# Kernel optimization log

Measured on AMD Instinct MI355X. Metric: run time of the kernel, lower is better.

The kernel has to match this reference:

```python
import jax, jax.numpy as jnp
import numpy as np

B, C, HIMG, WIMG = 32, 3, 224, 224
P, D, L, F, H, NC = 16, 768, 12, 3072, 12, 1000
S = (HIMG // P) * (WIMG // P)  # 196 tokens
DH = D // H                    # 64 per head


def setup_inputs() -> dict:
    key = jax.random.key(0)
    ks = jax.random.split(key, 12)
    rn = lambda i, shape, sc: jax.random.normal(ks[i], shape, jnp.float32) * sc
    return dict(
        x=rn(0, (B, C, HIMG, WIMG), 1.0),
        conv_w=rn(1, (D, C, P, P), 0.02),
        conv_b=jnp.zeros((D,), jnp.float32),
        pos_embed=rn(2, (S, D), 0.02),
        ln1_s=jnp.ones((L, D), jnp.float32),
        ln1_b=jnp.zeros((L, D), jnp.float32),
        wq=rn(3, (L, D, D), 0.02),
        wk=rn(4, (L, D, D), 0.02),
        wv=rn(5, (L, D, D), 0.02),
        ln2_s=jnp.ones((L, D), jnp.float32),
        ln2_b=jnp.zeros((L, D), jnp.float32),
        w1=rn(6, (L, D, F), 0.02),
        b1=jnp.zeros((L, F), jnp.float32),
        w2=rn(7, (L, F, D), 0.02),
        b2=jnp.zeros((L, D), jnp.float32),
        fc_w=rn(8, (D, NC), 0.02),
        fc_b=jnp.zeros((NC,), jnp.float32),
    )


def _layernorm(x, scale, bias, eps=1e-5):
    m = x.mean(-1, keepdims=True)
    v = ((x - m) ** 2).mean(-1, keepdims=True)
    return (x - m) * jax.lax.rsqrt(v + eps) * scale + bias


def reference(x, conv_w, conv_b, pos_embed, ln1_s, ln1_b, wq, wk, wv,
              ln2_s, ln2_b, w1, b1, w2, b2, fc_w, fc_b):
    # patch embedding: stride-P conv, then b c h w -> b (h w) c, add pos embed
    h = jax.lax.conv_general_dilated(
        x, conv_w, (P, P), 'VALID',
        dimension_numbers=('NCHW', 'OIHW', 'NCHW'))
    h = h + conv_b[None, :, None, None]
    h = h.reshape(B, D, S).transpose(0, 2, 1) + pos_embed  # [B,S,D]

    # NOTE: original scales attention logits by 1/sqrt(seq_len), not 1/sqrt(d_head)
    scale = 1.0 / jnp.sqrt(jnp.float32(S))

    def layer(hx, p):
        l1s, l1b, Wq, Wk, Wv, l2s, l2b, W1, B1, W2, B2 = p
        xn = _layernorm(hx, l1s, l1b)
        q = (xn @ Wq).reshape(B, S, H, DH)
        k = (xn @ Wk).reshape(B, S, H, DH)
        v = (xn @ Wv).reshape(B, S, H, DH)
        att = jax.nn.softmax(jnp.einsum('bshd,bthd->bhst', q, k) * scale, axis=-1)
        o = jnp.einsum('bhst,bthd->bshd', att, v).reshape(B, S, D)
        hx = hx + o
        y = _layernorm(hx, l2s, l2b) @ W1 + B1
        y = jax.nn.gelu(y, approximate=False) @ W2 + B2
        return hx + y, None

    h, _ = jax.lax.scan(layer, h, (ln1_s, ln1_b, wq, wk, wv,
                                   ln2_s, ln2_b, w1, b1, w2, b2))
    return h.mean(axis=1) @ fc_w + fc_b  # [B, num_classes]
```

## Files before the change

### kernel.cpp

```cpp
#include <hip/hip_runtime.h>
#include <hip/hip_bf16.h>

typedef __attribute__((ext_vector_type(8))) short bf16x8;
typedef __attribute__((ext_vector_type(4))) short bf16x4;
typedef __attribute__((ext_vector_type(4))) float f32x4;

#define DEVI static __device__ __forceinline__

DEVI unsigned short f2bf(float f) {
  __hip_bfloat16 h = __float2bfloat16(f);
  return __builtin_bit_cast(unsigned short, h);
}

DEVI f32x4 mfma16(bf16x8 a, bf16x8 b, f32x4 c) {
  return __builtin_amdgcn_mfma_f32_16x16x32_bf16(a, b, c, 0, 0, 0);
}

DEVI void gload16(const unsigned short* g, unsigned short* l) {
  __builtin_amdgcn_global_load_lds(
      (const __attribute__((address_space(1))) void*)g,
      (__attribute__((address_space(3))) void*)l, 16, 0, 0);
}

DEVI float erf_fast(float x) {
  float ax = fabsf(x);
  float t = 1.f / (1.f + 0.3275911f * ax);
  float poly = ((((1.061405429f * t - 1.453152027f) * t + 1.421413741f) * t -
                 0.284496736f) * t + 0.254829592f) * t;
  float e = __expf(-x * x);
  float er = 1.f - poly * e;
  return copysignf(er, x);
}

__global__ __launch_bounds__(256) void k_im2col(const float* __restrict__ x,
                                                unsigned short* __restrict__ A) {
  int t = blockIdx.x * 256 + threadIdx.x;
  int m = t / 192;
  int qq = t - m * 192;
  int kk = qq * 4;
  int c = kk >> 8;
  int r = kk & 255;
  int i = r >> 4;
  int j = r & 15;
  int b = m / 196;
  int s = m - b * 196;
  int ph = s / 14;
  int pw = s - ph * 14;
  const float* src = x + ((size_t)((b * 3 + c) * 224 + ph * 16 + i)) * 224 + pw * 16 + j;
  f32x4 v = *reinterpret_cast<const f32x4*>(src);
  bf16x4 o;
  o[0] = (short)f2bf(v[0]); o[1] = (short)f2bf(v[1]);
  o[2] = (short)f2bf(v[2]); o[3] = (short)f2bf(v[3]);
  *reinterpret_cast<bf16x4*>(A + (size_t)m * 768 + kk) = o;
}

__global__ __launch_bounds__(256) void k_cvt(const float* __restrict__ in,
                                             unsigned short* __restrict__ out) {
  int t = blockIdx.x * 256 + threadIdx.x;
  f32x4 v = *reinterpret_cast<const f32x4*>(in + (size_t)t * 4);
  bf16x4 o;
  o[0] = (short)f2bf(v[0]); o[1] = (short)f2bf(v[1]);
  o[2] = (short)f2bf(v[2]); o[3] = (short)f2bf(v[3]);
  *reinterpret_cast<bf16x4*>(out + (size_t)t * 4) = o;
}

DEVI void transpose_tile(const float* __restrict__ in, unsigned short* __restrict__ out,
                         int K, int N, int kt, int nt, unsigned short (*tile)[68]) {
  int r = threadIdx.x >> 4;
  int c4 = (threadIdx.x & 15) * 4;
  int k0 = kt * 64, n0 = nt * 64;
#pragma unroll
  for (int rr0 = 0; rr0 < 4; rr0++) {
    int rr = r + rr0 * 16;
    f32x4 v = *reinterpret_cast<const f32x4*>(in + (size_t)(k0 + rr) * N + n0 + c4);
    bf16x4 o;
    o[0] = (short)f2bf(v[0]); o[1] = (short)f2bf(v[1]);
    o[2] = (short)f2bf(v[2]); o[3] = (short)f2bf(v[3]);
    *reinterpret_cast<bf16x4*>(&tile[rr][c4]) = o;
  }
  __syncthreads();
#pragma unroll
  for (int rr0 = 0; rr0 < 4; rr0++) {
    int rr = r + rr0 * 16;
    bf16x4 o;
    o[0] = (short)tile[c4 + 0][rr];
    o[1] = (short)tile[c4 + 1][rr];
    o[2] = (short)tile[c4 + 2][rr];
    o[3] = (short)tile[c4 + 3][rr];
    *reinterpret_cast<bf16x4*>(out + (size_t)(n0 + rr) * K + k0 + c4) = o;
  }
}

__global__ __launch_bounds__(256) void k_wconvert(
    const float* __restrict__ wq, const float* __restrict__ wk, const float* __restrict__ wv,
    const float* __restrict__ w1, const float* __restrict__ w2,
    unsigned short* __restrict__ wqkvT, unsigned short* __restrict__ w1T,
    unsigned short* __restrict__ w2T) {
  __shared__ unsigned short tile[64][68];
  int bid = blockIdx.x;
  if (bid < 432) {
    int mm = bid / 144, t2 = bid - mm * 144;
    const float* in = (mm == 0) ? wq : ((mm == 1) ? wk : wv);
    transpose_tile(in, wqkvT + (size_t)mm * 768 * 768, 768, 768, t2 / 12, t2 % 12, tile);
  } else if (bid < 1008) {
    int t2 = bid - 432;
    transpose_tile(w1, w1T, 768, 3072, t2 / 48, t2 % 48, tile);
  } else {
    int t2 = bid - 1008;
    transpose_tile(w2, w2T, 3072, 768, t2 / 12, t2 % 12, tile);
  }
}

__global__ __launch_bounds__(256) void k_ln(const float* __restrict__ h,
                                            const float* __restrict__ sc,
                                            const float* __restrict__ bi,
                                            unsigned short* __restrict__ xn) {
  int wave = threadIdx.x >> 6, lane = threadIdx.x & 63;
  int row = blockIdx.x * 4 + wave;
  const float* hr = h + (size_t)row * 768;
  f32x4 v[3];
  float sum = 0.f;
#pragma unroll
  for (int i = 0; i < 3; i++) {
    v[i] = *reinterpret_cast<const f32x4*>(hr + i * 256 + lane * 4);
    sum += v[i][0] + v[i][1] + v[i][2] + v[i][3];
  }
#pragma unroll
  for (int m = 1; m < 64; m <<= 1) sum += __shfl_xor(sum, m, 64);
  float mean = sum * (1.f / 768.f);
  float var = 0.f;
#pragma unroll
  for (int i = 0; i < 3; i++)
#pragma unroll
    for (int c = 0; c < 4; c++) { float d = v[i][c] - mean; var += d * d; }
#pragma unroll
  for (int m = 1; m < 64; m <<= 1) var += __shfl_xor(var, m, 64);
  float rs = rsqrtf(var * (1.f / 768.f) + 1e-5f);
#pragma unroll
  for (int i = 0; i < 3; i++) {
    int col = i * 256 + lane * 4;
    f32x4 s4 = *reinterpret_cast<const f32x4*>(sc + col);
    f32x4 b4 = *reinterpret_cast<const f32x4*>(bi + col);
    bf16x4 o;
#pragma unroll
    for (int c = 0; c < 4; c++) o[c] = (short)f2bf((v[i][c] - mean) * rs * s4[c] + b4[c]);
    *reinterpret_cast<bf16x4*>(xn + (size_t)row * 768 + col) = o;
  }
}

template <int EPI>
__global__ __launch_bounds__(256) void k_gemm(
    const unsigned short* __restrict__ A, const unsigned short* __restrict__ Bt, int K,
    const float* __restrict__ bias, const float* __restrict__ aux,
    float* __restrict__ outF, unsigned short* __restrict__ outB) {
  __shared__ __align__(16) unsigned short As[2][128 * 32];
  __shared__ __align__(16) unsigned short Bs[2][128 * 32];

  int GX = gridDim.x, GY = gridDim.y;
  int nb = GX * GY;
  int lin = blockIdx.y * GX + blockIdx.x;
  int q = nb >> 3, r8 = nb & 7;
  int xcd = lin & 7, off = lin >> 3;
  int wid = (xcd < r8 ? xcd * (q + 1) : r8 * (q + 1) + (xcd - r8) * q) + off;
  const int GM = 8;
  int per = GM * GX;
  int g = wid / per;
  int first_m = g * GM;
  int gm = min(GM, GY - first_m);
  int rem = wid - g * per;
  int mt = first_m + rem % gm;
  int nt = rem / gm;
  int m0 = mt * 128, n0 = nt * 128;

  int tid = threadIdx.x;
  int wave = tid >> 6, lane = tid & 63;
  int wm = (wave >> 1) * 64, wn = (wave & 1) * 64;
  int lr = lane & 15, lg = lane >> 4;

  f32x4 acc[4][4];
  const f32x4 fz = {0.f, 0.f, 0.f, 0.f};
#pragma unroll
  for (int i = 0; i < 4; i++)
#pragma unroll
    for (int j = 0; j < 4; j++) acc[i][j] = fz;

  int srow = wave * 16 + (lane >> 2);
  int scol = (lane & 3) * 8;
  const unsigned short* Ag = A + (size_t)(m0 + srow) * K + scol;
  const unsigned short* Bg = Bt + (size_t)(n0 + srow) * K + scol;
  int lofs = wave * 16 * 32;

  int nk = K >> 5;
#pragma unroll
  for (int j = 0; j < 2; j++) {
    gload16(Ag + (size_t)j * 64 * K, &As[0][lofs + j * 64 * 32]);
    gload16(Bg + (size_t)j * 64 * K, &Bs[0][lofs + j * 64 * 32]);
  }
  __syncthreads();

  for (int kt = 0; kt < nk - 1; kt++) {
    int cur = kt & 1;
    int k0 = (kt + 1) << 5;
#pragma unroll
    for (int j = 0; j < 2; j++) {
      gload16(Ag + (size_t)j * 64 * K + k0, &As[cur ^ 1][lofs + j * 64 * 32]);
      gload16(Bg + (size_t)j * 64 * K + k0, &Bs[cur ^ 1][lofs + j * 64 * 32]);
    }
    bf16x8 a[4], b[4];
#pragma unroll
    for (int i = 0; i < 4; i++) {
      a[i] = *reinterpret_cast<const bf16x8*>(&As[cur][(wm + i * 16 + lr) * 32 + lg * 8]);
      b[i] = *reinterpret_cast<const bf16x8*>(&Bs[cur][(wn + i * 16 + lr) * 32 + lg * 8]);
    }
#pragma unroll
    for (int mi = 0; mi < 4; mi++)
#pragma unroll
      for (int ni = 0; ni < 4; ni++) acc[mi][ni] = mfma16(a[mi], b[ni], acc[mi][ni]);
    __syncthreads();
  }
  {
    int cur = (nk - 1) & 1;
    bf16x8 a[4], b[4];
#pragma unroll
    for (int i = 0; i < 4; i++) {
      a[i] = *reinterpret_cast<const bf16x8*>(&As[cur][(wm + i * 16 + lr) * 32 + lg * 8]);
      b[i] = *reinterpret_cast<const bf16x8*>(&Bs[cur][(wn + i * 16 + lr) * 32 + lg * 8]);
    }
#pragma unroll
    for (int mi = 0; mi < 4; mi++)
#pragma unroll
      for (int ni = 0; ni < 4; ni++) acc[mi][ni] = mfma16(a[mi], b[ni], acc[mi][ni]);
  }

  if (EPI == 1) {
#pragma unroll
    for (int ni = 0; ni < 4; ni++) {
      int n = n0 + wn + ni * 16 + lr;
      int which = (n >= 1536) ? 2 : ((n >= 768) ? 1 : 0);
      int n7 = n - which * 768;
      int hd = n7 >> 6, dh = n7 & 63;
      unsigned short* ob = outB + (size_t)which * 4816896 + dh;
#pragma unroll
      for (int mi = 0; mi < 4; mi++) {
        int mb = m0 + wm + mi * 16 + lg * 4;
        int bb = mb / 196;
        int s = mb - bb * 196;
#pragma unroll
        for (int r = 0; r < 4; r++) {
          ob[((size_t)((bb * 12 + hd) * 196 + s) << 6)] = f2bf(acc[mi][ni][r]);
          s++;
          if (s == 196) { s = 0; bb++; }
        }
      }
    }
  } else {
#pragma unroll
    for (int mi = 0; mi < 4; mi++) {
      int mb = m0 + wm + mi * 16 + lg * 4;
      int bb = mb / 196;
      int s0 = mb - bb * 196;
#pragma unroll
      for (int ni = 0; ni < 4; ni++) {
        int n = n0 + wn + ni * 16 + lr;
        int s = s0;
#pragma unroll
        for (int r = 0; r < 4; r++) {
          int m = mb + r;
          float val = acc[mi][ni][r];
          if (EPI == 0) {
            outF[(size_t)m * 768 + n] = val + bias[n] + aux[(size_t)s * 768 + n];
            s++;
            if (s == 196) s = 0;
          } else if (EPI == 2) {
            float u = val + bias[n];
            float gg = 0.5f * u * (1.f + erf_fast(u * 0.70710678118654752f));
            outB[(size_t)m * 3072 + n] = f2bf(gg);
          } else {
            outF[(size_t)m * 768 + n] += val + bias[n];
          }
        }
      }
    }
  }
}

__global__ __launch_bounds__(256) void k_attn(const unsigned short* __restrict__ q,
                                              const unsigned short* __restrict__ k,
                                              const unsigned short* __restrict__ v,
                                              float* __restrict__ h) {
  __shared__ __align__(16) unsigned short Kl[208][72];
  __shared__ __align__(16) unsigned short Vt[64][248];
  __shared__ __align__(16) unsigned short Sc[4][16][232];
  int bh = blockIdx.x;
  int b = bh / 12, hh = bh - b * 12;
  size_t base = (size_t)bh * 196 * 64;
  int tid = threadIdx.x, wave = tid >> 6, lane = tid & 63;
  int lr = lane & 15, lg = lane >> 4;

  const bf16x8 bz = {0, 0, 0, 0, 0, 0, 0, 0};
  for (int u = tid; u < 208 * 8; u += 256) {
    int row = u >> 3, c8 = (u & 7) * 8;
    bf16x8 val = bz;
    if (row < 196) val = *reinterpret_cast<const bf16x8*>(k + base + row * 64 + c8);
    *reinterpret_cast<bf16x8*>(&Kl[row][c8]) = val;
  }
  for (int u = tid; u < 224 * 8; u += 256) {
    int t = u >> 3, d8 = (u & 7) * 8;
    bf16x8 val = bz;
    if (t < 196) val = *reinterpret_cast<const bf16x8*>(v + base + t * 64 + d8);
#pragma unroll
    for (int i = 0; i < 8; i++) Vt[d8 + i][t] = (unsigned short)val[i];
  }
  for (int i2 = lane; i2 < 256; i2 += 64) Sc[wave][i2 >> 4][208 + (i2 & 15)] = 0;
  __syncthreads();

  const float scale = 1.f / 14.f;
  for (int st = wave; st < 13; st += 4) {
    int qb = st * 16;
    int s = qb + lr;
    bf16x8 aq0 = bz, aq1 = bz;
    if (s < 196) {
      aq0 = *reinterpret_cast<const bf16x8*>(q + base + (size_t)s * 64 + lg * 8);
      aq1 = *reinterpret_cast<const bf16x8*>(q + base + (size_t)s * 64 + 32 + lg * 8);
    }
    f32x4 sc[13];
#pragma unroll
    for (int t = 0; t < 13; t++) {
      bf16x8 bk0 = *reinterpret_cast<const bf16x8*>(&Kl[t * 16 + lr][lg * 8]);
      bf16x8 bk1 = *reinterpret_cast<const bf16x8*>(&Kl[t * 16 + lr][32 + lg * 8]);
      f32x4 z = {0.f, 0.f, 0.f, 0.f};
      z = mfma16(aq0, bk0, z);
      z = mfma16(aq1, bk1, z);
      sc[t] = z;
    }
    float mx[4] = {-1e30f, -1e30f, -1e30f, -1e30f};
#pragma unroll
    for (int t = 0; t < 13; t++) {
      int tc = t * 16 + lr;
#pragma unroll
      for (int r = 0; r < 4; r++) {
        float xv = (tc < 196) ? sc[t][r] * scale : -1e30f;
        sc[t][r] = xv;
        mx[r] = fmaxf(mx[r], xv);
      }
    }
#pragma unroll
    for (int r = 0; r < 4; r++)
#pragma unroll
      for (int mm = 1; mm < 16; mm <<= 1) mx[r] = fmaxf(mx[r], __shfl_xor(mx[r], mm, 64));
    float sm[4] = {0.f, 0.f, 0.f, 0.f};
#pragma unroll
    for (int t = 0; t < 13; t++)
#pragma unroll
      for (int r = 0; r < 4; r++) {
        float e = __expf(sc[t][r] - mx[r]);
        sc[t][r] = e;
        sm[r] += e;
      }
#pragma unroll
    for (int r = 0; r < 4; r++)
#pragma unroll
      for (int mm = 1; mm < 16; mm <<= 1) sm[r] += __shfl_xor(sm[r], mm, 64);
    float inv[4];
#pragma unroll
    for (int r = 0; r < 4; r++) inv[r] = 1.f / sm[r];
#pragma unroll
    for (int t = 0; t < 13; t++)
#pragma unroll
      for (int r = 0; r < 4; r++)
        Sc[wave][lg * 4 + r][t * 16 + lr] = f2bf(sc[t][r] * inv[r]);
    asm volatile("s_waitcnt lgkmcnt(0)" ::: "memory");
    bf16x8 ap[7];
#pragma unroll
    for (int ks = 0; ks < 7; ks++)
      ap[ks] = *reinterpret_cast<const bf16x8*>(&Sc[wave][lr][ks * 32 + lg * 8]);
#pragma unroll
    for (int nt = 0; nt < 4; nt++) {
      f32x4 o = {0.f, 0.f, 0.f, 0.f};
#pragma unroll
      for (int ks = 0; ks < 7; ks++) {
        bf16x8 bv = *reinterpret_cast<const bf16x8*>(&Vt[nt * 16 + lr][ks * 32 + lg * 8]);
        o = mfma16(ap[ks], bv, o);
      }
#pragma unroll
      for (int r = 0; r < 4; r++) {
        int s2 = qb + lg * 4 + r;
        if (s2 < 196) h[(size_t)(b * 196 + s2) * 768 + hh * 64 + nt * 16 + lr] += o[r];
      }
    }
  }
}

__global__ __launch_bounds__(256) void k_mean(const float* __restrict__ h,
                                              float* __restrict__ hm) {
  int b = blockIdx.x, d = blockIdx.y * 256 + threadIdx.x;
  float acc = 0.f;
  for (int s = 0; s < 196; s++) acc += h[(size_t)(b * 196 + s) * 768 + d];
  hm[b * 768 + d] = acc * (1.f / 196.f);
}

__global__ __launch_bounds__(256) void k_fc(const float* __restrict__ hm,
                                            const float* __restrict__ w,
                                            const float* __restrict__ bias,
                                            float* __restrict__ out) {
  int b = blockIdx.x, n = blockIdx.y * 256 + threadIdx.x;
  if (n >= 1000) return;
  float acc = bias[n];
  for (int d = 0; d < 768; d++) acc += hm[b * 768 + d] * w[d * 1000 + n];
  out[b * 1000 + n] = acc;
}

extern "C" void kernel_launch(void* const* d_in, const int* in_sizes, int n_in,
                              void* d_out, int out_size, void* d_ws, size_t ws_size,
                              hipStream_t stream) {
  const float* x      = (const float*)d_in[0];
  const float* conv_w = (const float*)d_in[1];
  const float* conv_b = (const float*)d_in[2];
  const float* pos    = (const float*)d_in[3];
  const float* ln1_s  = (const float*)d_in[4];
  const float* ln1_b  = (const float*)d_in[5];
  const float* wq     = (const float*)d_in[6];
  const float* wk     = (const float*)d_in[7];
  const float* wv     = (const float*)d_in[8];
  const float* ln2_s  = (const float*)d_in[9];
  const float* ln2_b  = (const float*)d_in[10];
  const float* w1     = (const float*)d_in[11];
  const float* b1     = (const float*)d_in[12];
  const float* w2     = (const float*)d_in[13];
  const float* b2     = (const float*)d_in[14];
  const float* fc_w   = (const float*)d_in[15];
  const float* fc_b   = (const float*)d_in[16];
  float* out = (float*)d_out;

  char* p = (char*)d_ws;
  auto alloc = [&](size_t bytes) {
    char* r = p;
    p += (bytes + 255) & ~(size_t)255;
    return r;
  };
  const size_t M = 6272, QSZ = 4816896;
  float* h              = (float*)alloc(M * 768 * 4);
  unsigned short* xn    = (unsigned short*)alloc(M * 768 * 2);
  unsigned short* qkv   = (unsigned short*)alloc(3 * QSZ * 2);
  unsigned short* y1    = (unsigned short*)alloc(M * 3072 * 2);
  unsigned short* wqkvT = (unsigned short*)alloc((size_t)2304 * 768 * 2);
  unsigned short* w1T   = (unsigned short*)alloc((size_t)3072 * 768 * 2);
  unsigned short* w2T   = (unsigned short*)alloc((size_t)3072 * 768 * 2);
  unsigned short* cwB   = (unsigned short*)alloc((size_t)768 * 768 * 2);
  float* hm             = (float*)alloc(32 * 768 * 4);

  k_cvt<<<576, 256, 0, stream>>>(conv_w, cwB);
  k_im2col<<<4704, 256, 0, stream>>>(x, xn);
  k_gemm<0><<<dim3(6, 49), 256, 0, stream>>>(xn, cwB, 768, conv_b, pos, h, nullptr);

  for (int l = 0; l < 12; l++) {
    k_wconvert<<<1584, 256, 0, stream>>>(
        wq + (size_t)l * 589824, wk + (size_t)l * 589824, wv + (size_t)l * 589824,
        w1 + (size_t)l * 2359296, w2 + (size_t)l * 2359296, wqkvT, w1T, w2T);
    k_ln<<<1568, 256, 0, stream>>>(h, ln1_s + l * 768, ln1_b + l * 768, xn);
    k_gemm<1><<<dim3(18, 49), 256, 0, stream>>>(xn, wqkvT, 768, nullptr, nullptr, nullptr, qkv);
    k_attn<<<384, 256, 0, stream>>>(qkv, qkv + QSZ, qkv + 2 * QSZ, h);
    k_ln<<<1568, 256, 0, stream>>>(h, ln2_s + l * 768, ln2_b + l * 768, xn);
    k_gemm<2><<<dim3(24, 49), 256, 0, stream>>>(xn, w1T, 768, b1 + (size_t)l * 3072, nullptr,
                                                nullptr, y1);
    k_gemm<3><<<dim3(6, 49), 256, 0, stream>>>(y1, w2T, 3072, b2 + (size_t)l * 768, nullptr, h,
                                               nullptr);
  }
  k_mean<<<dim3(32, 3), 256, 0, stream>>>(h, hm);
  k_fc<<<dim3(32, 4), 256, 0, stream>>>(hm, fc_w, fc_b, out);
}
```

Baseline: 3.274 ms.

## Add 256x256 tile GEMM with XCD-aware swizzle for QKV and MLP layers

Adds a new 512-thread GEMM kernel with 256x256 output tiles, 64-wide K steps, XOR-swizzled LDS layout, double-buffered direct global-to-LDS loads, and a block remap that groups tiles per XCD and by M-groups for L2 reuse. It is used for the QKV, FC1 and FC2 GEMMs, while the old kernel stays only for the patch embedding. Activation buffers are padded to 6400 rows so tiles can read past M without bounds checks, and the epilogue skips invalid rows. The larger tiles raise arithmetic intensity, at the cost of fewer blocks: FC2 gets only 75 blocks, which can underfill the GPU. The conv weight buffer now aliases the qkv buffer.

```diff
diff --git a/kernel.cpp b/kernel.cpp
--- a/kernel.cpp
+++ b/kernel.cpp
@@ -232,17 +232,140 @@
       for (int ni = 0; ni < 4; ni++) acc[mi][ni] = mfma16(a[mi], b[ni], acc[mi][ni]);
   }
 
-  if (EPI == 1) {
+#pragma unroll
+  for (int mi = 0; mi < 4; mi++) {
+    int mb = m0 + wm + mi * 16 + lg * 4;
+    int bb = mb / 196;
+    int s0 = mb - bb * 196;
 #pragma unroll
     for (int ni = 0; ni < 4; ni++) {
       int n = n0 + wn + ni * 16 + lr;
+      int s = s0;
+#pragma unroll
+      for (int r = 0; r < 4; r++) {
+        int m = mb + r;
+        float val = acc[mi][ni][r];
+        outF[(size_t)m * 768 + n] = val + bias[n] + aux[(size_t)s * 768 + n];
+        s++;
+        if (s == 196) s = 0;
+      }
+    }
+  }
+}
+
+template <int EPI>
+__global__ __launch_bounds__(512) void k_gemm256(
+    const unsigned short* __restrict__ A, const unsigned short* __restrict__ Bt, int K,
+    const float* __restrict__ bias, float* __restrict__ outF,
+    unsigned short* __restrict__ outB) {
+  __shared__ __align__(16) unsigned short As[2][16384];
+  __shared__ __align__(16) unsigned short Bs[2][16384];
+  const int MVALID = 6272;
+
+  int GX = gridDim.x, GY = gridDim.y;
+  int nb = GX * GY;
+  int lin = blockIdx.y * GX + blockIdx.x;
+  int q = nb >> 3, r8 = nb & 7;
+  int xcd = lin & 7, off = lin >> 3;
+  int wid = (xcd < r8 ? xcd * (q + 1) : r8 * (q + 1) + (xcd - r8) * q) + off;
+  const int GM = 8;
+  int per = GM * GX;
+  int g = wid / per;
+  int first_m = g * GM;
+  int gm = min(GM, GY - first_m);
+  int rem = wid - g * per;
+  int mt = first_m + rem % gm;
+  int nt = rem / gm;
+  int m0 = mt * 256, n0 = nt * 256;
+
+  int tid = threadIdx.x;
+  int w = tid >> 6, lane = tid & 63;
+  int wm2 = w >> 2, wn4 = w & 3;
+  int lr = lane & 15, lg = lane >> 4;
+
+  f32x4 acc[8][4];
+  const f32x4 fz = {0.f, 0.f, 0.f, 0.f};
+#pragma unroll
+  for (int i = 0; i < 8; i++)
+#pragma unroll
+    for (int j = 0; j < 4; j++) acc[i][j] = fz;
+
+  int srow = w * 8 + (lane >> 3);
+  int scole = ((lane & 7) ^ (lane >> 3)) * 8;
+  const unsigned short* Ag = A + (size_t)(m0 + srow) * K + scole;
+  const unsigned short* Bg = Bt + (size_t)(n0 + srow) * K + scole;
+
+  int lofsA = wm2 * 8192 + lr * 64;
+  int lofsB = (wn4 >> 1) * 8192 + ((wn4 & 1) * 64 + lr) * 64;
+  int swz = (lr & 7) << 3;
+  int colk0 = (lg * 8) ^ swz;
+  int colk1 = (32 + lg * 8) ^ swz;
+
+  int nk = K >> 6;
+
+#define STAGE256(kt, buf)                                                      \
+  {                                                                            \
+    const unsigned short* a_ = Ag + (size_t)(kt) * 64;                         \
+    const unsigned short* b_ = Bg + (size_t)(kt) * 64;                         \
+    _Pragma("unroll") for (int h_ = 0; h_ < 2; h_++)                           \
+        _Pragma("unroll") for (int j_ = 0; j_ < 2; j_++) {                     \
+      size_t go_ = (size_t)(h_ * 128 + j_ * 64) * K;                           \
+      int lo_ = h_ * 8192 + (j_ * 8 + w) * 512;                                \
+      gload16(a_ + go_, &As[buf][lo_]);                                        \
+      gload16(b_ + go_, &Bs[buf][lo_]);                                        \
+    }                                                                          \
+  }
+
+#define COMPUTE256(buf)                                                        \
+  {                                                                            \
+    _Pragma("unroll") for (int ks = 0; ks < 2; ks++) {                         \
+      int ca = (ks == 0) ? colk0 : colk1;                                      \
+      bf16x8 bfr[4];                                                           \
+      _Pragma("unroll") for (int ni = 0; ni < 4; ni++) bfr[ni] =               \
+          *reinterpret_cast<const bf16x8*>(&Bs[buf][lofsB + ni * 1024 + ca]);  \
+      _Pragma("unroll") for (int mi = 0; mi < 8; mi++) {                       \
+        bf16x8 afr =                                                           \
+            *reinterpret_cast<const bf16x8*>(&As[buf][lofsA + mi * 1024 + ca]); \
+        _Pragma("unroll") for (int ni = 0; ni < 4; ni++) acc[mi][ni] =         \
+            mfma16(afr, bfr[ni], acc[mi][ni]);                                 \
+      }                                                                        \
+    }                                                                          \
+  }
+
+  STAGE256(0, 0);
+  STAGE256(1, 1);
+  asm volatile("s_waitcnt vmcnt(8)" ::: "memory");
+  __builtin_amdgcn_s_barrier();
+
+  for (int kt = 0; kt < nk; kt++) {
+    int cur = kt & 1;
+    COMPUTE256(cur);
+    asm volatile("s_waitcnt lgkmcnt(0)" ::: "memory");
+    __builtin_amdgcn_s_barrier();
+    if (kt + 2 < nk) {
+      STAGE256(kt + 2, cur);
+      asm volatile("s_waitcnt vmcnt(8)" ::: "memory");
+      __builtin_amdgcn_s_barrier();
+    } else if (kt + 1 < nk) {
+      asm volatile("s_waitcnt vmcnt(0)" ::: "memory");
+      __builtin_amdgcn_s_barrier();
+    }
+  }
+#undef STAGE256
+#undef COMPUTE256
+
+  if (EPI == 1) {
+#pragma unroll
+    for (int ni = 0; ni < 4; ni++) {
+      int n = n0 + wn4 * 64 + ni * 16 + lr;
       int which = (n >= 1536) ? 2 : ((n >= 768) ? 1 : 0);
       int n7 = n - which * 768;
       int hd = n7 >> 6, dh = n7 & 63;
       unsigned short* ob = outB + (size_t)which * 4816896 + dh;
 #pragma unroll
-      for (int mi = 0; mi < 4; mi++) {
-        int mb = m0 + wm + mi * 16 + lg * 4;
+      for (int mi = 0; mi < 8; mi++) {
+        int mb = m0 + wm2 * 128 + mi * 16 + lg * 4;
+        if (mb >= MVALID) continue;
         int bb = mb / 196;
         int s = mb - bb * 196;
 #pragma unroll
@@ -255,23 +378,17 @@
     }
   } else {
 #pragma unroll
-    for (int mi = 0; mi < 4; mi++) {
-      int mb = m0 + wm + mi * 16 + lg * 4;
-      int bb = mb / 196;
-      int s0 = mb - bb * 196;
+    for (int mi = 0; mi < 8; mi++) {
+      int mb = m0 + wm2 * 128 + mi * 16 + lg * 4;
+      if (mb >= MVALID) continue;
 #pragma unroll
       for (int ni = 0; ni < 4; ni++) {
-        int n = n0 + wn + ni * 16 + lr;
-        int s = s0;
+        int n = n0 + wn4 * 64 + ni * 16 + lr;
 #pragma unroll
         for (int r = 0; r < 4; r++) {
           int m = mb + r;
           float val = acc[mi][ni][r];
-          if (EPI == 0) {
-            outF[(size_t)m * 768 + n] = val + bias[n] + aux[(size_t)s * 768 + n];
-            s++;
-            if (s == 196) s = 0;
-          } else if (EPI == 2) {
+          if (EPI == 2) {
             float u = val + bias[n];
             float gg = 0.5f * u * (1.f + erf_fast(u * 0.70710678118654752f));
             outB[(size_t)m * 3072 + n] = f2bf(gg);
@@ -438,16 +555,16 @@
     p += (bytes + 255) & ~(size_t)255;
     return r;
   };
-  const size_t M = 6272, QSZ = 4816896;
+  const size_t M = 6272, MP = 6400, QSZ = 4816896;
   float* h              = (float*)alloc(M * 768 * 4);
-  unsigned short* xn    = (unsigned short*)alloc(M * 768 * 2);
+  unsigned short* xn    = (unsigned short*)alloc(MP * 768 * 2);
   unsigned short* qkv   = (unsigned short*)alloc(3 * QSZ * 2);
-  unsigned short* y1    = (unsigned short*)alloc(M * 3072 * 2);
+  unsigned short* y1    = (unsigned short*)alloc(MP * 3072 * 2);
   unsigned short* wqkvT = (unsigned short*)alloc((size_t)2304 * 768 * 2);
   unsigned short* w1T   = (unsigned short*)alloc((size_t)3072 * 768 * 2);
   unsigned short* w2T   = (unsigned short*)alloc((size_t)3072 * 768 * 2);
-  unsigned short* cwB   = (unsigned short*)alloc((size_t)768 * 768 * 2);
   float* hm             = (float*)alloc(32 * 768 * 4);
+  unsigned short* cwB   = qkv;
 
   k_cvt<<<576, 256, 0, stream>>>(conv_w, cwB);
   k_im2col<<<4704, 256, 0, stream>>>(x, xn);
@@ -458,13 +575,13 @@
         wq + (size_t)l * 589824, wk + (size_t)l * 589824, wv + (size_t)l * 589824,
         w1 + (size_t)l * 2359296, w2 + (size_t)l * 2359296, wqkvT, w1T, w2T);
     k_ln<<<1568, 256, 0, stream>>>(h, ln1_s + l * 768, ln1_b + l * 768, xn);
-    k_gemm<1><<<dim3(18, 49), 256, 0, stream>>>(xn, wqkvT, 768, nullptr, nullptr, nullptr, qkv);
+    k_gemm256<1><<<dim3(9, 25), 512, 0, stream>>>(xn, wqkvT, 768, nullptr, nullptr, qkv);
     k_attn<<<384, 256, 0, stream>>>(qkv, qkv + QSZ, qkv + 2 * QSZ, h);
     k_ln<<<1568, 256, 0, stream>>>(h, ln2_s + l * 768, ln2_b + l * 768, xn);
-    k_gemm<2><<<dim3(24, 49), 256, 0, stream>>>(xn, w1T, 768, b1 + (size_t)l * 3072, nullptr,
-                                                nullptr, y1);
-    k_gemm<3><<<dim3(6, 49), 256, 0, stream>>>(y1, w2T, 3072, b2 + (size_t)l * 768, nullptr, h,
-                                               nullptr);
+    k_gemm256<2><<<dim3(12, 25), 512, 0, stream>>>(xn, w1T, 768, b1 + (size_t)l * 3072,
+                                                   nullptr, y1);
+    k_gemm256<3><<<dim3(3, 25), 512, 0, stream>>>(y1, w2T, 3072, b2 + (size_t)l * 768, h,
+                                                  nullptr);
   }
   k_mean<<<dim3(32, 3), 256, 0, stream>>>(h, hm);
   k_fc<<<dim3(32, 4), 256, 0, stream>>>(hm, fc_w, fc_b, out);
```

New measurement: 3.572 ms. +9.1%, slower.

## Use 256x256 tiled GEMM with triple-buffered LDS and split-K atomics for MLP

Applied to the files above, without the earlier changes.

Replaces the 128x128 double-buffered GEMM for the QKV, FC1 and FC2 layers with a 512-thread, 256x256-tile kernel. It uses three LDS stages with explicit waitcnt and barrier control and raises wave priority around the MFMA block. Rows are padded to 6400 and the FC2 GEMM is split three ways along K, accumulating into the residual with atomicAdd. Larger tiles give more data reuse per load and the split restores parallelism for the narrow FC2 output. In exchange, atomics make FC2 accumulation order nondeterministic, padded rows do wasted work, and the larger tiles use more registers and LDS.

```diff
diff --git a/kernel.cpp b/kernel.cpp
--- a/kernel.cpp
+++ b/kernel.cpp
@@ -148,30 +148,14 @@
   }
 }
 
-template <int EPI>
-__global__ __launch_bounds__(256) void k_gemm(
+__global__ __launch_bounds__(256) void k_gemm_patch(
     const unsigned short* __restrict__ A, const unsigned short* __restrict__ Bt, int K,
     const float* __restrict__ bias, const float* __restrict__ aux,
-    float* __restrict__ outF, unsigned short* __restrict__ outB) {
+    float* __restrict__ outF) {
   __shared__ __align__(16) unsigned short As[2][128 * 32];
   __shared__ __align__(16) unsigned short Bs[2][128 * 32];
 
-  int GX = gridDim.x, GY = gridDim.y;
-  int nb = GX * GY;
-  int lin = blockIdx.y * GX + blockIdx.x;
-  int q = nb >> 3, r8 = nb & 7;
-  int xcd = lin & 7, off = lin >> 3;
-  int wid = (xcd < r8 ? xcd * (q + 1) : r8 * (q + 1) + (xcd - r8) * q) + off;
-  const int GM = 8;
-  int per = GM * GX;
-  int g = wid / per;
-  int first_m = g * GM;
-  int gm = min(GM, GY - first_m);
-  int rem = wid - g * per;
-  int mt = first_m + rem % gm;
-  int nt = rem / gm;
-  int m0 = mt * 128, n0 = nt * 128;
-
+  int m0 = blockIdx.y * 128, n0 = blockIdx.x * 128;
   int tid = threadIdx.x;
   int wave = tid >> 6, lane = tid & 63;
   int wm = (wave >> 1) * 64, wn = (wave & 1) * 64;
@@ -232,17 +216,136 @@
       for (int ni = 0; ni < 4; ni++) acc[mi][ni] = mfma16(a[mi], b[ni], acc[mi][ni]);
   }
 
-  if (EPI == 1) {
+#pragma unroll
+  for (int mi = 0; mi < 4; mi++) {
+    int mb = m0 + wm + mi * 16 + lg * 4;
+    int bb = mb / 196;
+    int s0 = mb - bb * 196;
 #pragma unroll
     for (int ni = 0; ni < 4; ni++) {
       int n = n0 + wn + ni * 16 + lr;
+      int s = s0;
+#pragma unroll
+      for (int r = 0; r < 4; r++) {
+        int m = mb + r;
+        outF[(size_t)m * 768 + n] = acc[mi][ni][r] + bias[n] + aux[(size_t)s * 768 + n];
+        s++;
+        if (s == 196) s = 0;
+      }
+    }
+  }
+}
+
+template <int EPI>
+__global__ __launch_bounds__(512) void k_gemm256(
+    const unsigned short* __restrict__ A, const unsigned short* __restrict__ Bt,
+    int K, int nk, const float* __restrict__ bias, float* __restrict__ outF,
+    unsigned short* __restrict__ outB) {
+  __shared__ __align__(16) unsigned short As[3][8192];
+  __shared__ __align__(16) unsigned short Bs[3][8192];
+  const int MVALID = 6272;
+
+  int GX = gridDim.x, GY = gridDim.y, GZ = gridDim.z;
+  int nb = GX * GY * GZ;
+  int lin = (blockIdx.z * GY + blockIdx.y) * GX + blockIdx.x;
+  int q = nb >> 3, r8 = nb & 7;
+  int xcd = lin & 7, off = lin >> 3;
+  int wid = (xcd < r8 ? xcd * (q + 1) : r8 * (q + 1) + (xcd - r8) * q) + off;
+  int t2 = GX * GY;
+  int sz = wid / t2;
+  int w2 = wid - sz * t2;
+  const int GM = 4;
+  int per = GM * GX;
+  int g = w2 / per;
+  int first_m = g * GM;
+  int gm = min(GM, GY - first_m);
+  int rem = w2 - g * per;
+  int mt = first_m + rem % gm;
+  int nt = rem / gm;
+  int m0 = mt * 256, n0 = nt * 256;
+  int kb = sz * nk;
+
+  int tid = threadIdx.x;
+  int w = tid >> 6, lane = tid & 63;
+  int wm2 = w >> 2, wn4 = w & 3;
+  int lr = lane & 15, lg = lane >> 4;
+
+  f32x4 acc[8][4];
+  const f32x4 fz = {0.f, 0.f, 0.f, 0.f};
+#pragma unroll
+  for (int i = 0; i < 8; i++)
+#pragma unroll
+    for (int j = 0; j < 4; j++) acc[i][j] = fz;
+
+  const unsigned short* Ag =
+      A + (size_t)(m0 + (lane >> 2)) * K + (lane & 3) * 8 + (size_t)kb * 32;
+  const unsigned short* Bg =
+      Bt + (size_t)(n0 + (lane >> 2)) * K + (lane & 3) * 8 + (size_t)kb * 32;
+
+  int lofsA = wm2 * 4096 + lr * 32 + lg * 8;
+  int lofsB = wn4 * 2048 + lr * 32 + lg * 8;
+
+#define STAGE32(kt, la, lb)                                                    \
+  {                                                                            \
+    const unsigned short* a_ = Ag + (size_t)(kt) * 32;                         \
+    const unsigned short* b_ = Bg + (size_t)(kt) * 32;                         \
+    gload16(a_ + (size_t)w * 16 * K, (la) + w * 512);                          \
+    gload16(a_ + (size_t)(w + 8) * 16 * K, (la) + (w + 8) * 512);              \
+    gload16(b_ + (size_t)w * 16 * K, (lb) + w * 512);                          \
+    gload16(b_ + (size_t)(w + 8) * 16 * K, (lb) + (w + 8) * 512);              \
+  }
+
+#define COMPUTE32(pa, pb)                                                      \
+  {                                                                            \
+    bf16x8 afr[8], bfr[4];                                                     \
+    _Pragma("unroll") for (int ni = 0; ni < 4; ni++) bfr[ni] =                 \
+        *reinterpret_cast<const bf16x8*>((pb) + lofsB + ni * 512);             \
+    _Pragma("unroll") for (int mi = 0; mi < 8; mi++) afr[mi] =                 \
+        *reinterpret_cast<const bf16x8*>((pa) + lofsA + mi * 512);             \
+    __builtin_amdgcn_s_setprio(1);                                             \
+    _Pragma("unroll") for (int mi = 0; mi < 8; mi++)                           \
+        _Pragma("unroll") for (int ni = 0; ni < 4; ni++) acc[mi][ni] =         \
+            mfma16(afr[mi], bfr[ni], acc[mi][ni]);                             \
+    __builtin_amdgcn_s_setprio(0);                                             \
+  }
+
+  unsigned short* pa0 = &As[0][0]; unsigned short* pb0 = &Bs[0][0];
+  unsigned short* pa1 = &As[1][0]; unsigned short* pb1 = &Bs[1][0];
+  unsigned short* pa2 = &As[2][0]; unsigned short* pb2 = &Bs[2][0];
+
+  STAGE32(0, pa0, pb0);
+  STAGE32(1, pa1, pb1);
+
+  for (int kt = 0; kt < nk - 1; kt++) {
+    asm volatile("s_waitcnt lgkmcnt(0)" ::: "memory");
+    asm volatile("s_waitcnt vmcnt(4)" ::: "memory");
+    __builtin_amdgcn_s_barrier();
+    __builtin_amdgcn_sched_barrier(0);
+    if (kt + 2 < nk) STAGE32(kt + 2, pa2, pb2);
+    COMPUTE32(pa0, pb0);
+    unsigned short* ta = pa0; pa0 = pa1; pa1 = pa2; pa2 = ta;
+    unsigned short* tb = pb0; pb0 = pb1; pb1 = pb2; pb2 = tb;
+  }
+  asm volatile("s_waitcnt lgkmcnt(0)" ::: "memory");
+  asm volatile("s_waitcnt vmcnt(0)" ::: "memory");
+  __builtin_amdgcn_s_barrier();
+  __builtin_amdgcn_sched_barrier(0);
+  COMPUTE32(pa0, pb0);
+#undef STAGE32
+#undef COMPUTE32
+
+  if (EPI == 1) {
+#pragma unroll
+    for (int ni = 0; ni < 4; ni++) {
+      int n = n0 + wn4 * 64 + ni * 16 + lr;
       int which = (n >= 1536) ? 2 : ((n >= 768) ? 1 : 0);
       int n7 = n - which * 768;
       int hd = n7 >> 6, dh = n7 & 63;
       unsigned short* ob = outB + (size_t)which * 4816896 + dh;
 #pragma unroll
-      for (int mi = 0; mi < 4; mi++) {
-        int mb = m0 + wm + mi * 16 + lg * 4;
+      for (int mi = 0; mi < 8; mi++) {
+        int mb = m0 + wm2 * 128 + mi * 16 + lg * 4;
+        if (mb >= MVALID) continue;
         int bb = mb / 196;
         int s = mb - bb * 196;
 #pragma unroll
@@ -255,28 +358,23 @@
     }
   } else {
 #pragma unroll
-    for (int mi = 0; mi < 4; mi++) {
-      int mb = m0 + wm + mi * 16 + lg * 4;
-      int bb = mb / 196;
-      int s0 = mb - bb * 196;
+    for (int mi = 0; mi < 8; mi++) {
+      int mb = m0 + wm2 * 128 + mi * 16 + lg * 4;
+      if (mb >= MVALID) continue;
 #pragma unroll
       for (int ni = 0; ni < 4; ni++) {
-        int n = n0 + wn + ni * 16 + lr;
-        int s = s0;
+        int n = n0 + wn4 * 64 + ni * 16 + lr;
 #pragma unroll
         for (int r = 0; r < 4; r++) {
           int m = mb + r;
           float val = acc[mi][ni][r];
-          if (EPI == 0) {
-            outF[(size_t)m * 768 + n] = val + bias[n] + aux[(size_t)s * 768 + n];
-            s++;
-            if (s == 196) s = 0;
-          } else if (EPI == 2) {
+          if (EPI == 2) {
             float u = val + bias[n];
             float gg = 0.5f * u * (1.f + erf_fast(u * 0.70710678118654752f));
             outB[(size_t)m * 3072 + n] = f2bf(gg);
           } else {
-            outF[(size_t)m * 768 + n] += val + bias[n];
+            float bn = (sz == 0) ? bias[n] : 0.f;
+            atomicAdd(&outF[(size_t)m * 768 + n], val + bn);
           }
         }
       }
@@ -438,33 +536,34 @@
     p += (bytes + 255) & ~(size_t)255;
     return r;
   };
-  const size_t M = 6272, QSZ = 4816896;
+  const size_t M = 6272, MP = 6400, QSZ = 4816896;
   float* h              = (float*)alloc(M * 768 * 4);
-  unsigned short* xn    = (unsigned short*)alloc(M * 768 * 2);
+  unsigned short* xn    = (unsigned short*)alloc(MP * 768 * 2);
   unsigned short* qkv   = (unsigned short*)alloc(3 * QSZ * 2);
-  unsigned short* y1    = (unsigned short*)alloc(M * 3072 * 2);
+  unsigned short* y1    = (unsigned short*)alloc(MP * 3072 * 2);
   unsigned short* wqkvT = (unsigned short*)alloc((size_t)2304 * 768 * 2);
   unsigned short* w1T   = (unsigned short*)alloc((size_t)3072 * 768 * 2);
   unsigned short* w2T   = (unsigned short*)alloc((size_t)3072 * 768 * 2);
-  unsigned short* cwB   = (unsigned short*)alloc((size_t)768 * 768 * 2);
   float* hm             = (float*)alloc(32 * 768 * 4);
+  unsigned short* cwB   = qkv;
 
   k_cvt<<<576, 256, 0, stream>>>(conv_w, cwB);
   k_im2col<<<4704, 256, 0, stream>>>(x, xn);
-  k_gemm<0><<<dim3(6, 49), 256, 0, stream>>>(xn, cwB, 768, conv_b, pos, h, nullptr);
+  k_gemm_patch<<<dim3(6, 49), 256, 0, stream>>>(xn, cwB, 768, conv_b, pos, h);
 
   for (int l = 0; l < 12; l++) {
     k_wconvert<<<1584, 256, 0, stream>>>(
         wq + (size_t)l * 589824, wk + (size_t)l * 589824, wv + (size_t)l * 589824,
         w1 + (size_t)l * 2359296, w2 + (size_t)l * 2359296, wqkvT, w1T, w2T);
     k_ln<<<1568, 256, 0, stream>>>(h, ln1_s + l * 768, ln1_b + l * 768, xn);
-    k_gemm<1><<<dim3(18, 49), 256, 0, stream>>>(xn, wqkvT, 768, nullptr, nullptr, nullptr, qkv);
+    k_gemm256<1><<<dim3(9, 25, 1), 512, 0, stream>>>(xn, wqkvT, 768, 24, nullptr, nullptr,
+                                                     qkv);
     k_attn<<<384, 256, 0, stream>>>(qkv, qkv + QSZ, qkv + 2 * QSZ, h);
     k_ln<<<1568, 256, 0, stream>>>(h, ln2_s + l * 768, ln2_b + l * 768, xn);
-    k_gemm<2><<<dim3(24, 49), 256, 0, stream>>>(xn, w1T, 768, b1 + (size_t)l * 3072, nullptr,
-                                                nullptr, y1);
-    k_gemm<3><<<dim3(6, 49), 256, 0, stream>>>(y1, w2T, 3072, b2 + (size_t)l * 768, nullptr, h,
-                                               nullptr);
+    k_gemm256<2><<<dim3(12, 25, 1), 512, 0, stream>>>(xn, w1T, 768, 24,
+                                                      b1 + (size_t)l * 3072, nullptr, y1);
+    k_gemm256<3><<<dim3(3, 25, 3), 512, 0, stream>>>(y1, w2T, 3072, 32,
+                                                     b2 + (size_t)l * 768, h, nullptr);
   }
   k_mean<<<dim3(32, 3), 256, 0, stream>>>(h, hm);
   k_fc<<<dim3(32, 4), 256, 0, stream>>>(hm, fc_w, fc_b, out);
```

Result: slower. 3.797 ms (+16.0%).

## Add 256x256 4-stage pipelined GEMM for QKV and FC1 projections

Applied to the files above, without the earlier changes.

Adds a new 512-thread GEMM kernel with 256x256 output tiles, a 4-deep global_load_lds ring buffer, swizzled LDS layout, XCD-aware block remapping with grouped M ordering, and s_setprio around the MFMA bursts. The QKV and FC1 GEMMs switch to it, and the original kernel keeps only the conv and FC2 epilogues. The xn and y1 buffers are padded to 6400 rows so the last M tile can read past the valid 6272 rows, and stores to those rows are skipped. The aim is more operand reuse per LDS load and better latency hiding. In exchange the kernel uses more registers and LDS and wastes some compute on padding rows. The conv weight buffer now aliases the qkv buffer.

```diff
diff --git a/kernel.cpp b/kernel.cpp
--- a/kernel.cpp
+++ b/kernel.cpp
@@ -232,17 +232,136 @@
       for (int ni = 0; ni < 4; ni++) acc[mi][ni] = mfma16(a[mi], b[ni], acc[mi][ni]);
   }
 
-  if (EPI == 1) {
+#pragma unroll
+  for (int mi = 0; mi < 4; mi++) {
+    int mb = m0 + wm + mi * 16 + lg * 4;
+    int bb = mb / 196;
+    int s0 = mb - bb * 196;
 #pragma unroll
     for (int ni = 0; ni < 4; ni++) {
       int n = n0 + wn + ni * 16 + lr;
+      int s = s0;
+#pragma unroll
+      for (int r = 0; r < 4; r++) {
+        int m = mb + r;
+        float val = acc[mi][ni][r];
+        if (EPI == 0) {
+          outF[(size_t)m * 768 + n] = val + bias[n] + aux[(size_t)s * 768 + n];
+          s++;
+          if (s == 196) s = 0;
+        } else {
+          outF[(size_t)m * 768 + n] += val + bias[n];
+        }
+      }
+    }
+  }
+}
+
+template <int EPI>
+__global__ __launch_bounds__(512, 2) void k_gemm256p(
+    const unsigned short* __restrict__ A, const unsigned short* __restrict__ Bt,
+    const float* __restrict__ bias, unsigned short* __restrict__ outB) {
+  const int K = 768, NK = 24;
+  __shared__ __align__(16) unsigned short LDS[4][16384];
+  const int MVALID = 6272;
+
+  int GX = gridDim.x, GY = gridDim.y;
+  int nb = GX * GY;
+  int lin = blockIdx.y * GX + blockIdx.x;
+  int q = nb >> 3, r8 = nb & 7;
+  int xcd = lin & 7, off = lin >> 3;
+  int wid = (xcd < r8 ? xcd * (q + 1) : r8 * (q + 1) + (xcd - r8) * q) + off;
+  const int GM = 4;
+  int per = GM * GX;
+  int g = wid / per;
+  int first_m = g * GM;
+  int gm = min(GM, GY - first_m);
+  int rem = wid - g * per;
+  int mt = first_m + rem % gm;
+  int nt = rem / gm;
+  int m0 = mt * 256, n0 = nt * 256;
+
+  int tid = threadIdx.x;
+  int w = tid >> 6, lane = tid & 63;
+  int wm = w >> 2, wn = w & 3;
+  int lr = lane & 15, lg = lane >> 4;
+
+  f32x4 acc[8][4];
+  const f32x4 fz = {0.f, 0.f, 0.f, 0.f};
+#pragma unroll
+  for (int i = 0; i < 8; i++)
+#pragma unroll
+    for (int j = 0; j < 4; j++) acc[i][j] = fz;
+
+  int srow = w * 16 + (lane >> 2);
+  int scol = ((lane & 3) ^ ((lane >> 3) & 3)) * 8;
+  const unsigned short* Ag = A + (size_t)(m0 + srow) * K + scol;
+  const unsigned short* Bg = Bt + (size_t)(n0 + srow) * K + scol;
+  int ldst = w * 512;
+
+  int colsw = (lg ^ ((lr >> 1) & 3)) * 8;
+  int rofA = wm * 4096 + lr * 32 + colsw;
+  int rofB = 8192 + wn * 2048 + lr * 32 + colsw;
+
+#define STAGEP(kt)                                                          \
+  {                                                                         \
+    unsigned short* d_ = &LDS[(kt) & 3][0];                                 \
+    const unsigned short* a_ = Ag + (kt) * 32;                              \
+    const unsigned short* b_ = Bg + (kt) * 32;                              \
+    gload16(a_, d_ + ldst);                                                 \
+    gload16(a_ + (size_t)128 * K, d_ + 4096 + ldst);                        \
+    gload16(b_, d_ + 8192 + ldst);                                          \
+    gload16(b_ + (size_t)128 * K, d_ + 12288 + ldst);                       \
+  }
+
+  STAGEP(0);
+  STAGEP(1);
+  STAGEP(2);
+  asm volatile("s_waitcnt vmcnt(8)" ::: "memory");
+  __builtin_amdgcn_s_barrier();
+
+  for (int kt = 0; kt < NK; kt++) {
+    if (kt + 3 < NK) STAGEP(kt + 3);
+    const unsigned short* bufA = &LDS[kt & 3][0];
+    bf16x8 a[8], b[4];
+#pragma unroll
+    for (int ni = 0; ni < 4; ni++)
+      b[ni] = *reinterpret_cast<const bf16x8*>(bufA + rofB + ni * 512);
+#pragma unroll
+    for (int mi = 0; mi < 8; mi++)
+      a[mi] = *reinterpret_cast<const bf16x8*>(bufA + rofA + mi * 512);
+    __builtin_amdgcn_s_setprio(1);
+#pragma unroll
+    for (int mi = 0; mi < 8; mi++)
+#pragma unroll
+      for (int ni = 0; ni < 4; ni++) acc[mi][ni] = mfma16(a[mi], b[ni], acc[mi][ni]);
+    __builtin_amdgcn_s_setprio(0);
+    if (kt + 1 < NK) {
+      asm volatile("s_waitcnt lgkmcnt(0)" ::: "memory");
+      if (kt + 3 < NK) {
+        asm volatile("s_waitcnt vmcnt(8)" ::: "memory");
+      } else if (kt + 2 < NK) {
+        asm volatile("s_waitcnt vmcnt(4)" ::: "memory");
+      } else {
+        asm volatile("s_waitcnt vmcnt(0)" ::: "memory");
+      }
+      __builtin_amdgcn_s_barrier();
+    }
+  }
+#undef STAGEP
+
+  if (EPI == 1) {
+#pragma unroll
+    for (int ni = 0; ni < 4; ni++) {
+      int n = n0 + wn * 64 + ni * 16 + lr;
       int which = (n >= 1536) ? 2 : ((n >= 768) ? 1 : 0);
       int n7 = n - which * 768;
       int hd = n7 >> 6, dh = n7 & 63;
       unsigned short* ob = outB + (size_t)which * 4816896 + dh;
 #pragma unroll
-      for (int mi = 0; mi < 4; mi++) {
-        int mb = m0 + wm + mi * 16 + lg * 4;
+      for (int mi = 0; mi < 8; mi++) {
+        int mb = m0 + wm * 128 + mi * 16 + lg * 4;
+        if (mb >= MVALID) continue;
         int bb = mb / 196;
         int s = mb - bb * 196;
 #pragma unroll
@@ -255,29 +374,18 @@
     }
   } else {
 #pragma unroll
-    for (int mi = 0; mi < 4; mi++) {
-      int mb = m0 + wm + mi * 16 + lg * 4;
-      int bb = mb / 196;
-      int s0 = mb - bb * 196;
+    for (int mi = 0; mi < 8; mi++) {
+      int mb = m0 + wm * 128 + mi * 16 + lg * 4;
+      if (mb >= MVALID) continue;
 #pragma unroll
       for (int ni = 0; ni < 4; ni++) {
-        int n = n0 + wn + ni * 16 + lr;
-        int s = s0;
+        int n = n0 + wn * 64 + ni * 16 + lr;
 #pragma unroll
         for (int r = 0; r < 4; r++) {
           int m = mb + r;
-          float val = acc[mi][ni][r];
-          if (EPI == 0) {
-            outF[(size_t)m * 768 + n] = val + bias[n] + aux[(size_t)s * 768 + n];
-            s++;
-            if (s == 196) s = 0;
-          } else if (EPI == 2) {
-            float u = val + bias[n];
-            float gg = 0.5f * u * (1.f + erf_fast(u * 0.70710678118654752f));
-            outB[(size_t)m * 3072 + n] = f2bf(gg);
-          } else {
-            outF[(size_t)m * 768 + n] += val + bias[n];
-          }
+          float u = acc[mi][ni][r] + bias[n];
+          float gg = 0.5f * u * (1.f + erf_fast(u * 0.70710678118654752f));
+          outB[(size_t)m * 3072 + n] = f2bf(gg);
         }
       }
     }
@@ -438,16 +546,16 @@
     p += (bytes + 255) & ~(size_t)255;
     return r;
   };
-  const size_t M = 6272, QSZ = 4816896;
+  const size_t M = 6272, MP = 6400, QSZ = 4816896;
   float* h              = (float*)alloc(M * 768 * 4);
-  unsigned short* xn    = (unsigned short*)alloc(M * 768 * 2);
+  unsigned short* xn    = (unsigned short*)alloc(MP * 768 * 2);
   unsigned short* qkv   = (unsigned short*)alloc(3 * QSZ * 2);
-  unsigned short* y1    = (unsigned short*)alloc(M * 3072 * 2);
+  unsigned short* y1    = (unsigned short*)alloc(MP * 3072 * 2);
   unsigned short* wqkvT = (unsigned short*)alloc((size_t)2304 * 768 * 2);
   unsigned short* w1T   = (unsigned short*)alloc((size_t)3072 * 768 * 2);
   unsigned short* w2T   = (unsigned short*)alloc((size_t)3072 * 768 * 2);
-  unsigned short* cwB   = (unsigned short*)alloc((size_t)768 * 768 * 2);
   float* hm             = (float*)alloc(32 * 768 * 4);
+  unsigned short* cwB   = qkv;
 
   k_cvt<<<576, 256, 0, stream>>>(conv_w, cwB);
   k_im2col<<<4704, 256, 0, stream>>>(x, xn);
@@ -458,13 +566,12 @@
         wq + (size_t)l * 589824, wk + (size_t)l * 589824, wv + (size_t)l * 589824,
         w1 + (size_t)l * 2359296, w2 + (size_t)l * 2359296, wqkvT, w1T, w2T);
     k_ln<<<1568, 256, 0, stream>>>(h, ln1_s + l * 768, ln1_b + l * 768, xn);
-    k_gemm<1><<<dim3(18, 49), 256, 0, stream>>>(xn, wqkvT, 768, nullptr, nullptr, nullptr, qkv);
+    k_gemm256p<1><<<dim3(9, 25), 512, 0, stream>>>(xn, wqkvT, nullptr, qkv);
     k_attn<<<384, 256, 0, stream>>>(qkv, qkv + QSZ, qkv + 2 * QSZ, h);
     k_ln<<<1568, 256, 0, stream>>>(h, ln2_s + l * 768, ln2_b + l * 768, xn);
-    k_gemm<2><<<dim3(24, 49), 256, 0, stream>>>(xn, w1T, 768, b1 + (size_t)l * 3072, nullptr,
-                                                nullptr, y1);
-    k_gemm<3><<<dim3(6, 49), 256, 0, stream>>>(y1, w2T, 3072, b2 + (size_t)l * 768, nullptr, h,
-                                               nullptr);
+    k_gemm256p<2><<<dim3(12, 25), 512, 0, stream>>>(xn, w1T, b1 + (size_t)l * 3072, y1);
+    k_gemm<3><<<dim3(6, 49), 256, 0, stream>>>(y1, w2T, 3072, b2 + (size_t)l * 768, nullptr,
+                                               h, nullptr);
   }
   k_mean<<<dim3(32, 3), 256, 0, stream>>>(h, hm);
   k_fc<<<dim3(32, 4), 256, 0, stream>>>(hm, fc_w, fc_b, out);
```

Result: no change. 3.266 ms (-0.2%).
